# Kernel optimization log

Measured on AMD Instinct MI355X. Metric: run time of the kernel, lower is better.

Reference implementation:

```python
import jax, jax.numpy as jnp
import numpy as np

N = 100000
E = 1600000
C = 64          # hidden_channels
F_IN = 3
F_OUT = 3
N_MP = 2        # message-passing layers


def _lin(k, fan_in, fan_out):
    kw, kb = jax.random.split(k)
    bound = 1.0 / np.sqrt(fan_in)
    W = jax.random.uniform(kw, (fan_in, fan_out), jnp.float32, -bound, bound)
    b = jax.random.uniform(kb, (fan_out,), jnp.float32, -bound, bound)
    return W, b


def setup_inputs() -> dict:
    key = jax.random.key(0)
    ks = jax.random.split(key, 32)
    x = jax.random.normal(ks[0], (N, F_IN), jnp.float32)
    pos = jax.random.normal(ks[1], (N, 3), jnp.float32)
    edge_index = jax.random.randint(ks[2], (2, E), 0, N, jnp.int64)

    enc_W0, enc_b0 = _lin(ks[3], F_IN, C)
    enc_W1, enc_b1 = _lin(ks[4], C, C)
    dec_W0, dec_b0 = _lin(ks[5], C, C)
    dec_W1, dec_b1 = _lin(ks[6], C, F_OUT)

    # stacked params for the N_MP message-passing layers
    eW0, eb0, eW1, eb1 = [], [], [], []
    nW0, nb0, nW1, nb1 = [], [], [], []
    for i in range(N_MP):
        W, b = _lin(ks[7 + 4 * i], 3 * C + 3, C); eW0.append(W); eb0.append(b)
        W, b = _lin(ks[8 + 4 * i], C, C);         eW1.append(W); eb1.append(b)
        W, b = _lin(ks[9 + 4 * i], 2 * C, C);     nW0.append(W); nb0.append(b)
        W, b = _lin(ks[10 + 4 * i], C, C);        nW1.append(W); nb1.append(b)
    stack = lambda xs: jnp.stack(xs, axis=0)
    return {
        "x": x, "pos": pos, "edge_index": edge_index,
        "enc_W0": enc_W0, "enc_b0": enc_b0, "enc_W1": enc_W1, "enc_b1": enc_b1,
        "dec_W0": dec_W0, "dec_b0": dec_b0, "dec_W1": dec_W1, "dec_b1": dec_b1,
        "mp_eW0": stack(eW0), "mp_eb0": stack(eb0),
        "mp_eW1": stack(eW1), "mp_eb1": stack(eb1),
        "mp_nW0": stack(nW0), "mp_nb0": stack(nb0),
        "mp_nW1": stack(nW1), "mp_nb1": stack(nb1),
    }


def reference(x, pos, edge_index,
              enc_W0, enc_b0, enc_W1, enc_b1,
              dec_W0, dec_b0, dec_W1, dec_b1,
              mp_eW0, mp_eb0, mp_eW1, mp_eb1,
              mp_nW0, mp_nb0, mp_nW1, mp_nb1):
    act = jax.nn.elu
    src, dst = edge_index[0], edge_index[1]

    # node encoder (2-layer MLP, activation between layers only)
    h = act(x @ enc_W0 + enc_b0)
    h = h @ enc_W1 + enc_b1

    pos_diff = pos[src] - pos[dst]  # [E, 3], constant across MP layers

    for i in range(N_MP):
        x_nei = h[src]               # [E, C]
        x_own = h[dst]               # [E, C]
        ea = jnp.concatenate([x_nei, x_own, x_nei - x_own, pos_diff], axis=1)
        ea = act(ea @ mp_eW0[i] + mp_eb0[i])
        ea = ea @ mp_eW1[i] + mp_eb1[i]
        # EdgeAggregation(aggr='add'): scatter-add edge features to target nodes
        agg = jax.ops.segment_sum(ea, dst, num_segments=N)  # [N, C]
        u = jnp.concatenate([h, agg], axis=1)                # [N, 2C]
        u = act(u @ mp_nW0[i] + mp_nb0[i])
        u = u @ mp_nW1[i] + mp_nb1[i]
        h = h + u  # residual

    # node decoder
    out = act(h @ dec_W0 + dec_b0)
    out = out @ dec_W1 + dec_b1
    return out
```

## Files before the change

### kernel.cpp

```cpp
#include <hip/hip_runtime.h>
#include <hip/hip_bf16.h>

#define NN 100000
#define NE 1600000
#define NBKT 391
#define BCAP 4608

typedef __hip_bfloat16 bf16;
typedef unsigned short u16;
typedef unsigned int u32;
typedef short bshort8 __attribute__((ext_vector_type(8)));
typedef float f32x4 __attribute__((ext_vector_type(4)));

__device__ __forceinline__ float b2f_raw(u16 u) {
    unsigned int w = ((unsigned int)u) << 16;
    float f; __builtin_memcpy(&f, &w, 4); return f;
}
__device__ __forceinline__ float uplo(u32 u) {
    u32 w = u << 16; float f; __builtin_memcpy(&f, &w, 4); return f;
}
__device__ __forceinline__ float uphi(u32 u) {
    u32 w = u & 0xFFFF0000u; float f; __builtin_memcpy(&f, &w, 4); return f;
}
__device__ __forceinline__ u16 f2bu(float f) {
    bf16 h = __float2bfloat16(f); u16 u; __builtin_memcpy(&u, &h, 2); return u;
}
__device__ __forceinline__ float eluf(float x) { return x > 0.f ? x : __expf(x) - 1.f; }

#define LOG2E 1.4426950408889634f
#define LN2F  0.6931471805599453f

#define OFF_ENC_W0 0
#define OFF_ENC_B0 192
#define OFF_ENC_W1 256
#define OFF_ENC_B1 4352
#define OFF_DEC_W0 4416
#define OFF_DEC_B0 8512
#define OFF_DEC_W1 8576
#define OFF_DEC_B1 8768
#define OFF_EW0    8832
#define OFF_EB0    33792
#define OFF_EW1    33920
#define OFF_EB1    42112
#define OFF_NW0    42240
#define OFF_NB0    58624
#define OFF_NW1    58752
#define OFF_NB1    66944
#define OFF_WF     67072
#define OFF_BFOLD  75264
#define WBLK_WORDS 75392

#define SWZ_V   12288
#define SWZ_N0  24576
#define SWZ_N1  45056
#define SWZ_DC  53248
#define SWZ_ENC 57344
#define SWZ_U16 61440

__global__ void probe_kernel(const u16* __restrict__ xr,
                             const unsigned int* __restrict__ er,
                             int* __restrict__ flags, int* __restrict__ gcursor) {
    int tid = threadIdx.x;
    gcursor[tid] = 0;
    if (tid >= 64) return;
    int lane = tid;
    int wild = 0, oddnz = 0;
#pragma unroll
    for (int k = 0; k < 4; ++k) {
        int e = (xr[lane + k * 64] >> 7) & 0xFF;
        if (e > 140 || (e < 90 && e != 0)) wild++;
    }
#pragma unroll
    for (int k = 0; k < 2; ++k)
        if (er[1 + 2 * (lane + k * 64)] != 0u) oddnz++;
#pragma unroll
    for (int off = 32; off; off >>= 1) {
        wild += __shfl_down(wild, off);
        oddnz += __shfl_down(oddnz, off);
    }
    if (lane == 0) { flags[0] = (wild > 16) ? 1 : 0; flags[1] = (oddnz < 8) ? 1 : 0; }
}

struct WPtrs { const void* p[16]; };

__global__ void canon_weights(WPtrs wp, float* __restrict__ wblk,
                              const int* __restrict__ flags) {
    const int offs[16] = {OFF_ENC_W0, OFF_ENC_B0, OFF_ENC_W1, OFF_ENC_B1,
                          OFF_DEC_W0, OFF_DEC_B0, OFF_DEC_W1, OFF_DEC_B1,
                          OFF_EW0, OFF_EB0, OFF_EW1, OFF_EB1,
                          OFF_NW0, OFF_NB0, OFF_NW1, OFF_NB1};
    const int ns[16]   = {192, 64, 4096, 64, 4096, 64, 192, 3,
                          24960, 128, 8192, 128, 16384, 128, 8192, 128};
    int t = blockIdx.y;
    int i = blockIdx.x * blockDim.x + threadIdx.x;
    if (i >= ns[t]) return;
    const void* s = wp.p[t];
    float v = flags[0] ? ((const float*)s)[i] : b2f_raw(((const u16*)s)[i]);
    wblk[offs[t] + i] = v;
}

__global__ void prep_wf(float* __restrict__ wblk) {
    int idx = blockIdx.x * 256 + threadIdx.x;
    if (idx < 8192) {
        int l = idx >> 12, r = idx & 4095, k = r >> 6, c = r & 63;
        const float* e1 = wblk + OFF_EW1 + l * 4096 + k * 64;
        const float* n0 = wblk + OFF_NW0 + l * 8192 + 64 * 64;
        float s = 0.f;
#pragma unroll 8
        for (int m = 0; m < 64; ++m) s += e1[m] * n0[m * 64 + c];
        wblk[OFF_WF + idx] = s;
    } else if (idx < 8320) {
        int i2 = idx - 8192;
        int l = i2 >> 6, c = i2 & 63;
        const float* b1 = wblk + OFF_EB1 + l * 64;
        const float* n0 = wblk + OFF_NW0 + l * 8192 + 64 * 64;
        float s = 0.f;
#pragma unroll 8
        for (int m = 0; m < 64; ++m) s += b1[m] * n0[m * 64 + c];
        wblk[OFF_BFOLD + i2] = s;
    }
}

__global__ void prep_swz(const float* __restrict__ wblk, u16* __restrict__ swz) {
    int t = blockIdx.x * 256 + threadIdx.x;
    if (t >= SWZ_U16) return;
    float v = 0.f;
    if (t < SWZ_N0) {
        int isV = (t >= SWZ_V);
        int t2 = isV ? t - SWZ_V : t;
        int l = t2 / 6144, r = t2 % 6144;
        int ks = r >> 11, nt = (r >> 9) & 3, lane = (r >> 3) & 63, j = r & 7;
        int k = ks * 32 + ((lane >> 4) & 3) * 8 + j;
        int n = nt * 16 + (lane & 15);
        const float* W = wblk + OFF_EW0 + l * 12480;
        if (k < 64)
            v = isV ? (W[(64 + k) * 64 + n] - W[(128 + k) * 64 + n])
                    : (W[k * 64 + n] + W[(128 + k) * 64 + n]);
        else if (k < 67) {
            v = W[(192 + (k - 64)) * 64 + n];
            if (isV) v = -v;
        }
    } else if (t < SWZ_N1) {
        int t2 = t - SWZ_N0;
        int l = t2 / 10240, r = t2 % 10240;
        int ks = r >> 11, nt = (r >> 9) & 3, lane = (r >> 3) & 63, j = r & 7;
        int k = ks * 32 + ((lane >> 4) & 3) * 8 + j;
        int n = nt * 16 + (lane & 15);
        if (k < 64)        v = wblk[OFF_NW0 + l * 8192 + k * 64 + n];
        else if (k < 128)  v = wblk[OFF_WF + l * 4096 + (k - 64) * 64 + n];
        else if (k == 128) v = wblk[OFF_BFOLD + l * 64 + n];
    } else if (t < SWZ_DC) {
        int t2 = t - SWZ_N1;
        int l = t2 / 4096, r = t2 % 4096;
        int ks = r >> 11, nt = (r >> 9) & 3, lane = (r >> 3) & 63, j = r & 7;
        int k = ks * 32 + ((lane >> 4) & 3) * 8 + j;
        int n = nt * 16 + (lane & 15);
        v = wblk[OFF_NW1 + l * 4096 + k * 64 + n];
    } else if (t < SWZ_ENC) {
        int r = t - SWZ_DC;
        int ks = r >> 11, nt = (r >> 9) & 3, lane = (r >> 3) & 63, j = r & 7;
        int k = ks * 32 + ((lane >> 4) & 3) * 8 + j;
        int n = nt * 16 + (lane & 15);
        v = wblk[OFF_DEC_W0 + k * 64 + n];
    } else {
        int r = t - SWZ_ENC;
        int ks = r >> 11, nt = (r >> 9) & 3, lane = (r >> 3) & 63, j = r & 7;
        int k = ks * 32 + ((lane >> 4) & 3) * 8 + j;
        int n = nt * 16 + (lane & 15);
        v = wblk[OFF_ENC_W1 + k * 64 + n];
    }
    swz[t] = f2bu(v);
}

__global__ __launch_bounds__(1024) void passA_bin(
    const void* __restrict__ eiraw, const int* __restrict__ flags,
    u32* __restrict__ epk_b, int* __restrict__ gcursor) {
    __shared__ int hist[NBKT];
    __shared__ int binstart[NBKT];
    __shared__ int gbase_l[NBKT];
    __shared__ int fill[NBKT];
    __shared__ int sc[512];
    __shared__ u32 stage[4096];
    __shared__ u16 slotbin[4096];
    int tid = threadIdx.x;
    for (int i = tid; i < NBKT; i += 1024) hist[i] = 0;
    __syncthreads();
    int base = blockIdx.x * 4096;
    int total = NE - base; if (total > 4096) total = 4096;
    bool i64 = flags[1] != 0;
    u32 ed[4]; int bn[4];
#pragma unroll
    for (int k = 0; k < 4; ++k) {
        int e = base + tid + k * 1024;
        bn[k] = -1;
        if (e < NE) {
            int s, d;
            if (i64) {
                s = (int)((const long long*)eiraw)[e];
                d = (int)((const long long*)eiraw)[(size_t)NE + e];
            } else {
                s = ((const int*)eiraw)[e];
                d = ((const int*)eiraw)[(size_t)NE + e];
            }
            if ((unsigned)s >= NN) s = 0;
            if ((unsigned)d >= NN) d = 0;
            ed[k] = (u32)s | ((u32)(d & 255) << 17);
            bn[k] = d >> 8;
            atomicAdd(&hist[bn[k]], 1);
        }
    }
    __syncthreads();
    if (tid < 512) sc[tid] = (tid < NBKT) ? hist[tid] : 0;
    __syncthreads();
    for (int d = 1; d < 512; d <<= 1) {
        int v = (tid >= d && tid < 512) ? sc[tid - d] : 0;
        __syncthreads();
        if (tid < 512) sc[tid] += v;
        __syncthreads();
    }
    if (tid < NBKT) {
        binstart[tid] = sc[tid] - hist[tid];
        fill[tid] = 0;
        gbase_l[tid] = hist[tid] ? atomicAdd(&gcursor[tid], hist[tid]) : 0;
    }
    __syncthreads();
#pragma unroll
    for (int k = 0; k < 4; ++k) {
        if (bn[k] >= 0) {
            int p = binstart[bn[k]] + atomicAdd(&fill[bn[k]], 1);
            stage[p] = ed[k];
            slotbin[p] = (u16)bn[k];
        }
    }
    __syncthreads();
    for (int i = tid; i < total; i += 1024) {
        int b = slotbin[i];
        int gp = gbase_l[b] + (i - binstart[b]);
        if (gp < BCAP) epk_b[(size_t)b * BCAP + gp] = stage[i];
    }
}

__global__ __launch_bounds__(512) void scan391(const int* __restrict__ gcursor,
                                               int* __restrict__ gbase2) {
    __shared__ int s[512];
    int t = threadIdx.x;
    int v = 0;
    if (t < NBKT) { v = gcursor[t]; if (v > BCAP) v = BCAP; }
    s[t] = v;
    __syncthreads();
    for (int d = 1; d < 512; d <<= 1) {
        int u = (t >= d) ? s[t - d] : 0;
        __syncthreads();
        s[t] += u;
        __syncthreads();
    }
    if (t < NBKT) gbase2[t] = s[t] - v;
}

__global__ __launch_bounds__(1024) void passB_sort(
    const u32* __restrict__ epk_b, const int* __restrict__ gcursor,
    const int* __restrict__ gbase2, int* __restrict__ srcs,
    int* __restrict__ start) {
    __shared__ int h256[256];
    __shared__ int off256[256];
    __shared__ int sc[256];
    __shared__ u32 stage[BCAP];
    int b = blockIdx.x, tid = threadIdx.x;
    int cnt = gcursor[b]; if (cnt > BCAP) cnt = BCAP;
    for (int i = tid; i < 256; i += 1024) h256[i] = 0;
    __syncthreads();
    u32 ed[5]; int dl[5];
#pragma unroll
    for (int k = 0; k < 5; ++k) {
        int i = tid + k * 1024;
        dl[k] = -1;
        if (i < cnt) {
            ed[k] = epk_b[(size_t)b * BCAP + i];
            dl[k] = (int)(ed[k] >> 17);
            atomicAdd(&h256[dl[k]], 1);
        }
    }
    __syncthreads();
    if (tid < 256) sc[tid] = h256[tid];
    __syncthreads();
    for (int d = 1; d < 256; d <<= 1) {
        int v = (tid >= d && tid < 256) ? sc[tid - d] : 0;
        __syncthreads();
        if (tid < 256) sc[tid] += v;
        __syncthreads();
    }
    int gb = gbase2[b];
    if (tid < 256) {
        off256[tid] = sc[tid] - h256[tid];
        start[b * 256 + tid] = gb + sc[tid] - h256[tid];
    }
    __syncthreads();
#pragma unroll
    for (int k = 0; k < 5; ++k) {
        if (dl[k] >= 0) {
            int p = atomicAdd(&off256[dl[k]], 1);
            stage[p] = ed[k];
        }
    }
    __syncthreads();
    for (int i = tid; i < cnt; i += 1024) srcs[gb + i] = (int)(stage[i] & 0x1FFFFu);
}

__global__ __launch_bounds__(512) void enc_uv(
    const void* __restrict__ xraw, const void* __restrict__ praw,
    const float* __restrict__ wblk, const u16* __restrict__ swzE,
    const u16* __restrict__ swzU, const u16* __restrict__ swzV,
    u16* __restrict__ hb, u16* __restrict__ pos4b,
    u16* __restrict__ U, u16* __restrict__ V,
    const int* __restrict__ flags) {
    __shared__ __attribute__((aligned(16))) u16 sE[4096];
    __shared__ __attribute__((aligned(16))) u16 sU[6144];
    __shared__ __attribute__((aligned(16))) u16 sV[6144];
    __shared__ __attribute__((aligned(16))) u16 sP[8][16 * 72];
    int tid = threadIdx.x;
    for (int i = tid; i < 512; i += 512) ((uint4*)sE)[i] = ((const uint4*)swzE)[i];
    for (int i = tid; i < 768; i += 512) {
        ((uint4*)sU)[i] = ((const uint4*)swzU)[i];
        ((uint4*)sV)[i] = ((const uint4*)swzV)[i];
    }
    __syncthreads();
    int wid = tid >> 6, lane = tid & 63;
    int m16 = lane & 15, half = lane >> 4;
    int g = blockIdx.x * 8 + wid;
    if (g >= NN / 16) return;
    int n0 = g * 16 + m16;
    bool isf = flags[0] != 0;
    float x0, x1, x2;
    if (isf) {
        x0 = ((const float*)xraw)[n0 * 3 + 0];
        x1 = ((const float*)xraw)[n0 * 3 + 1];
        x2 = ((const float*)xraw)[n0 * 3 + 2];
    } else {
        x0 = b2f_raw(((const u16*)xraw)[n0 * 3 + 0]);
        x1 = b2f_raw(((const u16*)xraw)[n0 * 3 + 1]);
        x2 = b2f_raw(((const u16*)xraw)[n0 * 3 + 2]);
    }
    u16 pk0 = 0, pk1 = 0, pk2 = 0;
    if (half == 0) {
        float p0 = isf ? ((const float*)praw)[n0 * 3 + 0] : b2f_raw(((const u16*)praw)[n0 * 3 + 0]);
        float p1 = isf ? ((const float*)praw)[n0 * 3 + 1] : b2f_raw(((const u16*)praw)[n0 * 3 + 1]);
        float p2 = isf ? ((const float*)praw)[n0 * 3 + 2] : b2f_raw(((const u16*)praw)[n0 * 3 + 2]);
        pk0 = f2bu(p0); pk1 = f2bu(p1); pk2 = f2bu(p2);
        *(ushort4*)(pos4b + (size_t)n0 * 4) = make_ushort4(pk0, pk1, pk2, 0);
    }
    const float* W0 = wblk + OFF_ENC_W0;
    const float* b0 = wblk + OFF_ENC_B0;
    bshort8 af0, af1;
#pragma unroll
    for (int j = 0; j < 8; ++j) {
        int c = half * 8 + j;
        float v = b0[c] + x0 * W0[c] + x1 * W0[64 + c] + x2 * W0[128 + c];
        af0[j] = (short)f2bu(eluf(v));
        int c2 = 32 + c;
        float v2 = b0[c2] + x0 * W0[c2] + x1 * W0[64 + c2] + x2 * W0[128 + c2];
        af1[j] = (short)f2bu(eluf(v2));
    }
    const bshort8* BE = (const bshort8*)sE;
    f32x4 acc[4];
#pragma unroll
    for (int nt = 0; nt < 4; ++nt) {
        float b = wblk[OFF_ENC_B1 + nt * 16 + m16];
        acc[nt] = f32x4{b, b, b, b};
    }
#pragma unroll
    for (int nt = 0; nt < 4; ++nt)
        acc[nt] = __builtin_amdgcn_mfma_f32_16x16x32_bf16(af0, BE[nt * 64 + lane], acc[nt], 0, 0, 0);
#pragma unroll
    for (int nt = 0; nt < 4; ++nt)
        acc[nt] = __builtin_amdgcn_mfma_f32_16x16x32_bf16(af1, BE[(4 + nt) * 64 + lane], acc[nt], 0, 0, 0);
    u16* myP = sP[wid];
#pragma unroll
    for (int nt = 0; nt < 4; ++nt)
#pragma unroll
        for (int r = 0; r < 4; ++r) {
            size_t ix = (size_t)(g * 16 + half * 4 + r) * 64 + nt * 16 + m16;
            u16 hv = f2bu(acc[nt][r]);
            hb[ix] = hv;
            myP[(half * 4 + r) * 72 + nt * 16 + m16] = hv;
        }
    bshort8 ah0 = *(const bshort8*)(myP + m16 * 72 + 0 * 32 + half * 8);
    bshort8 ah1 = *(const bshort8*)(myP + m16 * 72 + 1 * 32 + half * 8);
    bshort8 ap;
#pragma unroll
    for (int j = 0; j < 8; ++j) ap[j] = 0;
    if (half == 0) { ap[0] = (short)pk0; ap[1] = (short)pk1; ap[2] = (short)pk2; }
    const bshort8* BU = (const bshort8*)sU;
    const bshort8* BV = (const bshort8*)sV;
    const float* eb0p = wblk + OFF_EB0;
    f32x4 aU[4], aV[4];
#pragma unroll
    for (int nt = 0; nt < 4; ++nt) {
        float bv = eb0p[nt * 16 + m16];
        aU[nt] = f32x4{0.f, 0.f, 0.f, 0.f};
        aV[nt] = f32x4{bv, bv, bv, bv};
    }
#pragma unroll
    for (int nt = 0; nt < 4; ++nt) {
        aU[nt] = __builtin_amdgcn_mfma_f32_16x16x32_bf16(ah0, BU[nt * 64 + lane], aU[nt], 0, 0, 0);
        aV[nt] = __builtin_amdgcn_mfma_f32_16x16x32_bf16(ah0, BV[nt * 64 + lane], aV[nt], 0, 0, 0);
    }
#pragma unroll
    for (int nt = 0; nt < 4; ++nt) {
        aU[nt] = __builtin_amdgcn_mfma_f32_16x16x32_bf16(ah1, BU[(4 + nt) * 64 + lane], aU[nt], 0, 0, 0);
        aV[nt] = __builtin_amdgcn_mfma_f32_16x16x32_bf16(ah1, BV[(4 + nt) * 64 + lane], aV[nt], 0, 0, 0);
    }
#pragma unroll
    for (int nt = 0; nt < 4; ++nt) {
        aU[nt] = __builtin_amdgcn_mfma_f32_16x16x32_bf16(ap, BU[(8 + nt) * 64 + lane], aU[nt], 0, 0, 0);
        aV[nt] = __builtin_amdgcn_mfma_f32_16x16x32_bf16(ap, BV[(8 + nt) * 64 + lane], aV[nt], 0, 0, 0);
    }
#pragma unroll
    for (int nt = 0; nt < 4; ++nt)
#pragma unroll
        for (int r = 0; r < 4; ++r) {
            size_t ix = (size_t)(g * 16 + half * 4 + r) * 64 + nt * 16 + m16;
            U[ix] = f2bu(aU[nt][r] * LOG2E);
            V[ix] = f2bu(aV[nt][r] * LOG2E);
        }
}

#define ES_CAP 1024
__global__ __launch_bounds__(256) void edge_sum(
    const u32* __restrict__ U32, const u32* __restrict__ V32,
    const int* __restrict__ srcs, const int* __restrict__ start,
    u32* __restrict__ Sb, int totalwaves) {
    __shared__ int sS[4][ES_CAP];
    int tid = threadIdx.x;
    int wslot = tid >> 6;
    int w = blockIdx.x * 4 + wslot;
    int lane = tid & 63;
    int eo = lane >> 4, co = lane & 15;
    int nb = (int)((long long)w * NN / totalwaves);
    int ne = (int)((long long)(w + 1) * NN / totalwaves);
    int s0w = start[nb], s1w = start[ne];
    int cw = s1w - s0w;
    const int* sp = srcs + s0w;
    if (cw <= ES_CAP) {
        for (int i = lane; i < cw; i += 64) sS[wslot][i] = srcs[s0w + i];
        sp = sS[wslot];
    }
    __syncthreads();

    int s0 = s0w;
    for (int n = nb; n < ne; ++n) {
        int s1 = start[n + 1];
        int cnt = s1 - s0;
        const int* spn = sp + (s0 - s0w);
        uint2 vv = *(const uint2*)(V32 + (size_t)n * 32 + (co << 1));
        float v0 = uplo(vv.x), v1 = uphi(vv.x);
        float v2 = uplo(vv.y), v3 = uphi(vv.y);
        float accA0 = 0.f, accA1 = 0.f, accA2 = 0.f, accA3 = 0.f;
        float accB0 = 0.f, accB1 = 0.f, accB2 = 0.f, accB3 = 0.f;

        auto GRP = [&](int goff, bool MASKED) {
            int ei = goff + eo;
            int eic = ei;
            if (MASKED) eic = (ei < cnt) ? ei : (cnt - 1);
            int s = spn[eic];
            uint2 uu = *(const uint2*)(U32 + (size_t)s * 32 + (co << 1));
            float x0 = uplo(uu.x) + v0, x1 = uphi(uu.x) + v1;
            float x2 = uplo(uu.y) + v2, x3 = uphi(uu.y) + v3;
            float e0 = __builtin_amdgcn_exp2f(x0);
            float e1 = __builtin_amdgcn_exp2f(x1);
            float e2 = __builtin_amdgcn_exp2f(x2);
            float e3 = __builtin_amdgcn_exp2f(x3);
            bool val = !MASKED || (ei < cnt);
            accA0 += val ? fmaxf(x0, 0.f) : 0.f;
            accA1 += val ? fmaxf(x1, 0.f) : 0.f;
            accA2 += val ? fmaxf(x2, 0.f) : 0.f;
            accA3 += val ? fmaxf(x3, 0.f) : 0.f;
            accB0 += val ? fminf(e0, 1.f) : 0.f;
            accB1 += val ? fminf(e1, 1.f) : 0.f;
            accB2 += val ? fminf(e2, 1.f) : 0.f;
            accB3 += val ? fminf(e3, 1.f) : 0.f;
        };

        int g = 0;
        for (; g + 16 <= cnt; g += 16) {
            GRP(g + 0, false);
            GRP(g + 4, false);
            GRP(g + 8, false);
            GRP(g + 12, false);
        }
        int rem = cnt - g;
        if (rem > 0) {
            GRP(g + 0, true);
            if (rem > 4)  GRP(g + 4, true);
            if (rem > 8)  GRP(g + 8, true);
            if (rem > 12) GRP(g + 12, true);
        }

        float t0 = fmaf(accA0, LN2F, accB0);
        float t1 = fmaf(accA1, LN2F, accB1);
        float t2 = fmaf(accA2, LN2F, accB2);
        float t3 = fmaf(accA3, LN2F, accB3);
        t0 += __shfl_xor(t0, 16); t0 += __shfl_xor(t0, 32);
        t1 += __shfl_xor(t1, 16); t1 += __shfl_xor(t1, 32);
        t2 += __shfl_xor(t2, 16); t2 += __shfl_xor(t2, 32);
        t3 += __shfl_xor(t3, 16); t3 += __shfl_xor(t3, 32);
        if (eo == 0) {
            float cf = (float)cnt;
            u32 p0 = (u32)f2bu(t0 - cf) | ((u32)f2bu(t1 - cf) << 16);
            u32 p1 = (u32)f2bu(t2 - cf) | ((u32)f2bu(t3 - cf) << 16);
            *(uint2*)(Sb + (size_t)n * 32 + (co << 1)) = make_uint2(p0, p1);
        }
        s0 = s1;
    }
}

__global__ __launch_bounds__(512) void node_uv(
    u16* __restrict__ hb, const u16* __restrict__ Sb,
    const int* __restrict__ start, const float* __restrict__ wblk,
    const u16* __restrict__ swz, const u16* __restrict__ pos4b,
    u16* __restrict__ U, u16* __restrict__ V) {
    __shared__ __attribute__((aligned(16))) u16 sN0[10240];
    __shared__ __attribute__((aligned(16))) u16 sN1[4096];
    __shared__ __attribute__((aligned(16))) u16 sU[6144];
    __shared__ __attribute__((aligned(16))) u16 sV[6144];
    __shared__ __attribute__((aligned(16))) u16 sP[8][16 * 72];
    int tid = threadIdx.x;
    {
        const uint4* s0 = (const uint4*)(swz + SWZ_N0);
        const uint4* s1 = (const uint4*)(swz + SWZ_N1);
        const uint4* su = (const uint4*)(swz + 6144);
        const uint4* sv = (const uint4*)(swz + SWZ_V + 6144);
        for (int i = tid; i < 1280; i += 512) ((uint4*)sN0)[i] = s0[i];
        for (int i = tid; i < 512; i += 512)  ((uint4*)sN1)[i] = s1[i];
        for (int i = tid; i < 768; i += 512) {
            ((uint4*)sU)[i] = su[i];
            ((uint4*)sV)[i] = sv[i];
        }
    }
    __syncthreads();
    int wid = tid >> 6, lane = tid & 63;
    int m16 = lane & 15, half = lane >> 4;
    int g = blockIdx.x * 8 + wid;
    if (g >= NN / 16) return;
    int n0 = g * 16 + m16;
    const float* b0 = wblk + OFF_NB0;
    const float* b1 = wblk + OFF_NB1;
    const bshort8* B0 = (const bshort8*)sN0;
    const bshort8* B1 = (const bshort8*)sN1;
    u16* myP = sP[wid];

    bshort8 afh0 = *(const bshort8*)(hb + (size_t)n0 * 64 + half * 8);
    bshort8 afh1 = *(const bshort8*)(hb + (size_t)n0 * 64 + 32 + half * 8);
    bshort8 afs0 = *(const bshort8*)(Sb + (size_t)n0 * 64 + half * 8);
    bshort8 afs1 = *(const bshort8*)(Sb + (size_t)n0 * 64 + 32 + half * 8);
    bshort8 afd;
#pragma unroll
    for (int j = 0; j < 8; ++j) afd[j] = 0;
    if (half == 0) {
        float deg = (float)(start[n0 + 1] - start[n0]);
        afd[0] = (short)f2bu(deg);
    }
    f32x4 acc[4];
#pragma unroll
    for (int nt = 0; nt < 4; ++nt) {
        float b = b0[nt * 16 + m16];
        acc[nt] = f32x4{b, b, b, b};
    }
#pragma unroll
    for (int nt = 0; nt < 4; ++nt)
        acc[nt] = __builtin_amdgcn_mfma_f32_16x16x32_bf16(afh0, B0[nt * 64 + lane], acc[nt], 0, 0, 0);
#pragma unroll
    for (int nt = 0; nt < 4; ++nt)
        acc[nt] = __builtin_amdgcn_mfma_f32_16x16x32_bf16(afh1, B0[(4 + nt) * 64 + lane], acc[nt], 0, 0, 0);
#pragma unroll
    for (int nt = 0; nt < 4; ++nt)
        acc[nt] = __builtin_amdgcn_mfma_f32_16x16x32_bf16(afs0, B0[(8 + nt) * 64 + lane], acc[nt], 0, 0, 0);
#pragma unroll
    for (int nt = 0; nt < 4; ++nt)
        acc[nt] = __builtin_amdgcn_mfma_f32_16x16x32_bf16(afs1, B0[(12 + nt) * 64 + lane], acc[nt], 0, 0, 0);
#pragma unroll
    for (int nt = 0; nt < 4; ++nt)
        acc[nt] = __builtin_amdgcn_mfma_f32_16x16x32_bf16(afd, B0[(16 + nt) * 64 + lane], acc[nt], 0, 0, 0);
#pragma unroll
    for (int nt = 0; nt < 4; ++nt)
#pragma unroll
        for (int r = 0; r < 4; ++r) {
            float v = acc[nt][r];
            v = eluf(v);
            myP[(half * 4 + r) * 72 + nt * 16 + m16] = f2bu(v);
        }
    f32x4 acc2[4];
#pragma unroll
    for (int nt = 0; nt < 4; ++nt) {
        float b = b1[nt * 16 + m16];
        acc2[nt] = f32x4{b, b, b, b};
    }
#pragma unroll
    for (int ks = 0; ks < 2; ++ks) {
        bshort8 av = *(const bshort8*)(myP + m16 * 72 + ks * 32 + half * 8);
#pragma unroll
        for (int nt = 0; nt < 4; ++nt)
            acc2[nt] = __builtin_amdgcn_mfma_f32_16x16x32_bf16(
                av, B1[(ks * 4 + nt) * 64 + lane], acc2[nt], 0, 0, 0);
    }
#pragma unroll
    for (int nt = 0; nt < 4; ++nt)
#pragma unroll
        for (int r = 0; r < 4; ++r) {
            size_t ix = (size_t)(g * 16 + half * 4 + r) * 64 + nt * 16 + m16;
            float v = b2f_raw(hb[ix]) + acc2[nt][r];
            u16 hv = f2bu(v);
            hb[ix] = hv;
            myP[(half * 4 + r) * 72 + nt * 16 + m16] = hv;
        }
    bshort8 ah0 = *(const bshort8*)(myP + m16 * 72 + 0 * 32 + half * 8);
    bshort8 ah1 = *(const bshort8*)(myP + m16 * 72 + 1 * 32 + half * 8);
    bshort8 ap;
#pragma unroll
    for (int j = 0; j < 8; ++j) ap[j] = 0;
    if (half == 0) {
        ushort4 pp = *(const ushort4*)(pos4b + (size_t)n0 * 4);
        ap[0] = (short)pp.x; ap[1] = (short)pp.y; ap[2] = (short)pp.z;
    }
    const bshort8* BU = (const bshort8*)sU;
    const bshort8* BV = (const bshort8*)sV;
    const float* eb0p = wblk + OFF_EB0 + 64;
    f32x4 aU[4], aV[4];
#pragma unroll
    for (int nt = 0; nt < 4; ++nt) {
        float bv = eb0p[nt * 16 + m16];
        aU[nt] = f32x4{0.f, 0.f, 0.f, 0.f};
        aV[nt] = f32x4{bv, bv, bv, bv};
    }
#pragma unroll
    for (int nt = 0; nt < 4; ++nt) {
        aU[nt] = __builtin_amdgcn_mfma_f32_16x16x32_bf16(ah0, BU[nt * 64 + lane], aU[nt], 0, 0, 0);
        aV[nt] = __builtin_amdgcn_mfma_f32_16x16x32_bf16(ah0, BV[nt * 64 + lane], aV[nt], 0, 0, 0);
    }
#pragma unroll
    for (int nt = 0; nt < 4; ++nt) {
        aU[nt] = __builtin_amdgcn_mfma_f32_16x16x32_bf16(ah1, BU[(4 + nt) * 64 + lane], aU[nt], 0, 0, 0);
        aV[nt] = __builtin_amdgcn_mfma_f32_16x16x32_bf16(ah1, BV[(4 + nt) * 64 + lane], aV[nt], 0, 0, 0);
    }
#pragma unroll
    for (int nt = 0; nt < 4; ++nt) {
        aU[nt] = __builtin_amdgcn_mfma_f32_16x16x32_bf16(ap, BU[(8 + nt) * 64 + lane], aU[nt], 0, 0, 0);
        aV[nt] = __builtin_amdgcn_mfma_f32_16x16x32_bf16(ap, BV[(8 + nt) * 64 + lane], aV[nt], 0, 0, 0);
    }
#pragma unroll
    for (int nt = 0; nt < 4; ++nt)
#pragma unroll
        for (int r = 0; r < 4; ++r) {
            size_t ix = (size_t)(g * 16 + half * 4 + r) * 64 + nt * 16 + m16;
            U[ix] = f2bu(aU[nt][r] * LOG2E);
            V[ix] = f2bu(aV[nt][r] * LOG2E);
        }
}

__global__ __launch_bounds__(512) void node_dec(
    const u16* __restrict__ hb, const u16* __restrict__ Sb,
    const int* __restrict__ start, const float* __restrict__ wblk,
    const u16* __restrict__ swz,
    void* __restrict__ out, const int* __restrict__ flags) {
    __shared__ __attribute__((aligned(16))) u16 sN0[10240];
    __shared__ __attribute__((aligned(16))) u16 sN1[4096];
    __shared__ __attribute__((aligned(16))) u16 sDec[4096];
    __shared__ __attribute__((aligned(16))) float sT[8][1048];
    int tid = threadIdx.x;
    {
        const uint4* s0 = (const uint4*)(swz + SWZ_N0 + 10240);
        const uint4* s1 = (const uint4*)(swz + SWZ_N1 + 4096);
        const uint4* sd = (const uint4*)(swz + SWZ_DC);
        for (int i = tid; i < 1280; i += 512) ((uint4*)sN0)[i] = s0[i];
        for (int i = tid; i < 512; i += 512)  ((uint4*)sN1)[i] = s1[i];
        for (int i = tid; i < 512; i += 512)  ((uint4*)sDec)[i] = sd[i];
    }
    __syncthreads();
    int wid = tid >> 6, lane = tid & 63;
    int m16 = lane & 15, half = lane >> 4;
    int g = blockIdx.x * 8 + wid;
    if (g >= NN / 16) return;
    int n0 = g * 16 + m16;
    const float* b0 = wblk + OFF_NB0 + 64;
    const float* b1 = wblk + OFF_NB1 + 64;
    const bshort8* B0 = (const bshort8*)sN0;
    const bshort8* B1 = (const bshort8*)sN1;
    const bshort8* BD = (const bshort8*)sDec;
    u16* myP = (u16*)sT[wid];
    float* sD = sT[wid];

    bshort8 afh0 = *(const bshort8*)(hb + (size_t)n0 * 64 + half * 8);
    bshort8 afh1 = *(const bshort8*)(hb + (size_t)n0 * 64 + 32 + half * 8);
    bshort8 afs0 = *(const bshort8*)(Sb + (size_t)n0 * 64 + half * 8);
    bshort8 afs1 = *(const bshort8*)(Sb + (size_t)n0 * 64 + 32 + half * 8);
    bshort8 afd;
#pragma unroll
    for (int j = 0; j < 8; ++j) afd[j] = 0;
    if (half == 0) {
        float deg = (float)(start[n0 + 1] - start[n0]);
        afd[0] = (short)f2bu(deg);
    }
    f32x4 acc[4];
#pragma unroll
    for (int nt = 0; nt < 4; ++nt) {
        float b = b0[nt * 16 + m16];
        acc[nt] = f32x4{b, b, b, b};
    }
#pragma unroll
    for (int nt = 0; nt < 4; ++nt)
        acc[nt] = __builtin_amdgcn_mfma_f32_16x16x32_bf16(afh0, B0[nt * 64 + lane], acc[nt], 0, 0, 0);
#pragma unroll
    for (int nt = 0; nt < 4; ++nt)
        acc[nt] = __builtin_amdgcn_mfma_f32_16x16x32_bf16(afh1, B0[(4 + nt) * 64 + lane], acc[nt], 0, 0, 0);
#pragma unroll
    for (int nt = 0; nt < 4; ++nt)
        acc[nt] = __builtin_amdgcn_mfma_f32_16x16x32_bf16(afs0, B0[(8 + nt) * 64 + lane], acc[nt], 0, 0, 0);
#pragma unroll
    for (int nt = 0; nt < 4; ++nt)
        acc[nt] = __builtin_amdgcn_mfma_f32_16x16x32_bf16(afs1, B0[(12 + nt) * 64 + lane], acc[nt], 0, 0, 0);
#pragma unroll
    for (int nt = 0; nt < 4; ++nt)
        acc[nt] = __builtin_amdgcn_mfma_f32_16x16x32_bf16(afd, B0[(16 + nt) * 64 + lane], acc[nt], 0, 0, 0);
#pragma unroll
    for (int nt = 0; nt < 4; ++nt)
#pragma unroll
        for (int r = 0; r < 4; ++r) {
            float v = acc[nt][r];
            v = eluf(v);
            myP[(half * 4 + r) * 72 + nt * 16 + m16] = f2bu(v);
        }
    f32x4 acc2[4];
#pragma unroll
    for (int nt = 0; nt < 4; ++nt) {
        float b = b1[nt * 16 + m16];
        acc2[nt] = f32x4{b, b, b, b};
    }
#pragma unroll
    for (int ks = 0; ks < 2; ++ks) {
        bshort8 av = *(const bshort8*)(myP + m16 * 72 + ks * 32 + half * 8);
#pragma unroll
        for (int nt = 0; nt < 4; ++nt)
            acc2[nt] = __builtin_amdgcn_mfma_f32_16x16x32_bf16(
                av, B1[(ks * 4 + nt) * 64 + lane], acc2[nt], 0, 0, 0);
    }
    float nh[4][4];
#pragma unroll
    for (int nt = 0; nt < 4; ++nt)
#pragma unroll
        for (int r = 0; r < 4; ++r) {
            size_t ix = (size_t)(g * 16 + half * 4 + r) * 64 + nt * 16 + m16;
            nh[nt][r] = b2f_raw(hb[ix]) + acc2[nt][r];
        }
#pragma unroll
    for (int nt = 0; nt < 4; ++nt)
#pragma unroll
        for (int r = 0; r < 4; ++r)
            myP[(half * 4 + r) * 72 + nt * 16 + m16] = f2bu(nh[nt][r]);
    const float* db0 = wblk + OFF_DEC_B0;
    f32x4 acc3[4];
#pragma unroll
    for (int nt = 0; nt < 4; ++nt) {
        float b = db0[nt * 16 + m16];
        acc3[nt] = f32x4{b, b, b, b};
    }
#pragma unroll
    for (int ks = 0; ks < 2; ++ks) {
        bshort8 av = *(const bshort8*)(myP + m16 * 72 + ks * 32 + half * 8);
#pragma unroll
        for (int nt = 0; nt < 4; ++nt)
            acc3[nt] = __builtin_amdgcn_mfma_f32_16x16x32_bf16(
                av, BD[(ks * 4 + nt) * 64 + lane], acc3[nt], 0, 0, 0);
    }
#pragma unroll
    for (int nt = 0; nt < 4; ++nt)
#pragma unroll
        for (int r = 0; r < 4; ++r) {
            float v = acc3[nt][r];
            v = eluf(v);
            sD[(half * 4 + r) * 65 + nt * 16 + m16] = v;
        }
    if (lane < 48) {
        int j = lane / 3, o = lane - j * 3;
        const float* dW1 = wblk + OFF_DEC_W1;
        float oacc = wblk[OFF_DEC_B1 + o];
#pragma unroll
        for (int k = 0; k < 64; ++k) oacc += sD[j * 65 + k] * dW1[k * 3 + o];
        int nn = g * 16 + j;
        if (flags[0]) ((float*)out)[nn * 3 + o] = oacc;
        else          ((bf16*)out)[nn * 3 + o] = __float2bfloat16(oacc);
    }
}

extern "C" void kernel_launch(void* const* d_in, const int* in_sizes, int n_in,
                              void* d_out, int out_size, void* d_ws, size_t ws_size,
                              hipStream_t stream) {
    int*   flags   = (int*)d_ws;
    float* wblk    = (float*)d_ws + 16;
    u16*   swz     = (u16*)(wblk + WBLK_WORDS);
    u16*   pos4b   = swz + SWZ_U16;
    int*   gcursor = (int*)(pos4b + 400000);
    int*   gbase2  = gcursor + 512;
    int*   start   = gbase2 + 512;
    int*   srcs    = start + NN + 512;
    u16*   Sb      = (u16*)(srcs + NE);
    u16*   hb      = Sb + (size_t)NN * 64;
    u16*   U       = hb + (size_t)NN * 64;
    u16*   V       = U + (size_t)NN * 64;
    u32*   epk_b   = (u32*)Sb;

    probe_kernel<<<1, 512, 0, stream>>>((const u16*)d_in[0],
                                        (const unsigned int*)d_in[2], flags, gcursor);

    WPtrs wp;
    wp.p[0] = d_in[3];  wp.p[1] = d_in[4];  wp.p[2] = d_in[5];  wp.p[3] = d_in[6];
    wp.p[4] = d_in[7];  wp.p[5] = d_in[8];  wp.p[6] = d_in[9];  wp.p[7] = d_in[10];
    wp.p[8] = d_in[11]; wp.p[9] = d_in[12]; wp.p[10] = d_in[13]; wp.p[11] = d_in[14];
    wp.p[12] = d_in[15]; wp.p[13] = d_in[16]; wp.p[14] = d_in[17]; wp.p[15] = d_in[18];
    canon_weights<<<dim3(98, 16), 256, 0, stream>>>(wp, wblk, flags);
    prep_wf<<<33, 256, 0, stream>>>(wblk);
    prep_swz<<<240, 256, 0, stream>>>(wblk, swz);

    passA_bin<<<(NE + 4095) / 4096, 1024, 0, stream>>>(d_in[2], flags, epk_b, gcursor);
    scan391<<<1, 512, 0, stream>>>(gcursor, gbase2);
    passB_sort<<<NBKT, 1024, 0, stream>>>(epk_b, gcursor, gbase2, srcs, start);

    const int NODE_BLOCKS = (NN / 16 + 7) / 8;
    const int EDGE_BLOCKS = 2048;
    const int TOTALWAVES = EDGE_BLOCKS * 4;

    enc_uv<<<NODE_BLOCKS, 512, 0, stream>>>(
        d_in[0], d_in[1], wblk, swz + SWZ_ENC,
        swz, swz + SWZ_V, hb, pos4b, U, V, flags);

    edge_sum<<<EDGE_BLOCKS, 256, 0, stream>>>(
        (const u32*)U, (const u32*)V, srcs, start, (u32*)Sb, TOTALWAVES);
    node_uv<<<NODE_BLOCKS, 512, 0, stream>>>(
        hb, Sb, start, wblk, swz, pos4b, U, V);

    edge_sum<<<EDGE_BLOCKS, 256, 0, stream>>>(
        (const u32*)U, (const u32*)V, srcs, start, (u32*)Sb, TOTALWAVES);
    node_dec<<<NODE_BLOCKS, 512, 0, stream>>>(
        hb, Sb, start, wblk, swz, d_out, flags);
}
```

Before: 314.5 us.

## Software-prefetch next node's sources in edge_sum instead of LDS staging

Removes the per-wave LDS staging of source indices and the block-wide barrier in edge_sum. Instead, each wave prefetches the first 16 source indices and the V row for the next node while it processes the current one. The block count doubles and launch bounds now request higher occupancy. This trades one LDS copy plus a sync for a register-level software pipeline over dependent global loads. Edges past the first 16 now read their indices straight from global memory, and the prefetch can read slightly past a node's segment.

```diff
diff --git a/kernel.cpp b/kernel.cpp
--- a/kernel.cpp
+++ b/kernel.cpp
@@ -424,81 +424,101 @@
         }
 }
 
-#define ES_CAP 1024
-__global__ __launch_bounds__(256) void edge_sum(
+__global__ __launch_bounds__(256, 8) void edge_sum(
     const u32* __restrict__ U32, const u32* __restrict__ V32,
     const int* __restrict__ srcs, const int* __restrict__ start,
     u32* __restrict__ Sb, int totalwaves) {
-    __shared__ int sS[4][ES_CAP];
     int tid = threadIdx.x;
-    int wslot = tid >> 6;
-    int w = blockIdx.x * 4 + wslot;
+    int w = blockIdx.x * 4 + (tid >> 6);
     int lane = tid & 63;
     int eo = lane >> 4, co = lane & 15;
+    int coff = co << 1;
     int nb = (int)((long long)w * NN / totalwaves);
     int ne = (int)((long long)(w + 1) * NN / totalwaves);
-    int s0w = start[nb], s1w = start[ne];
-    int cw = s1w - s0w;
-    const int* sp = srcs + s0w;
-    if (cw <= ES_CAP) {
-        for (int i = lane; i < cw; i += 64) sS[wslot][i] = srcs[s0w + i];
-        sp = sS[wslot];
-    }
-    __syncthreads();
-
-    int s0 = s0w;
+    if (nb >= ne) return;
+
+    int s0 = start[nb];
+    int s1 = start[nb + 1];
+    int pf0 = srcs[s0 + eo];
+    int pf1 = srcs[s0 + 4 + eo];
+    int pf2 = srcs[s0 + 8 + eo];
+    int pf3 = srcs[s0 + 12 + eo];
+    uint2 pv = *(const uint2*)(V32 + (size_t)nb * 32 + coff);
+
     for (int n = nb; n < ne; ++n) {
-        int s1 = start[n + 1];
         int cnt = s1 - s0;
-        const int* spn = sp + (s0 - s0w);
-        uint2 vv = *(const uint2*)(V32 + (size_t)n * 32 + (co << 1));
+        int sv0 = pf0, sv1 = pf1, sv2 = pf2, sv3 = pf3;
+        uint2 vv = pv;
+        int s0n = s1;
+        int s1n = start[n + 2];
+        {
+            int vn = (n + 1 < NN) ? (n + 1) : (NN - 1);
+            pf0 = srcs[s0n + eo];
+            pf1 = srcs[s0n + 4 + eo];
+            pf2 = srcs[s0n + 8 + eo];
+            pf3 = srcs[s0n + 12 + eo];
+            pv = *(const uint2*)(V32 + (size_t)vn * 32 + coff);
+        }
+
         float v0 = uplo(vv.x), v1 = uphi(vv.x);
         float v2 = uplo(vv.y), v3 = uphi(vv.y);
-        float accA0 = 0.f, accA1 = 0.f, accA2 = 0.f, accA3 = 0.f;
-        float accB0 = 0.f, accB1 = 0.f, accB2 = 0.f, accB3 = 0.f;
-
-        auto GRP = [&](int goff, bool MASKED) {
-            int ei = goff + eo;
-            int eic = ei;
-            if (MASKED) eic = (ei < cnt) ? ei : (cnt - 1);
-            int s = spn[eic];
-            uint2 uu = *(const uint2*)(U32 + (size_t)s * 32 + (co << 1));
+        float aA0 = 0.f, aA1 = 0.f, aA2 = 0.f, aA3 = 0.f;
+        float aB0 = 0.f, aB1 = 0.f, aB2 = 0.f, aB3 = 0.f;
+
+        auto body = [&](uint2 uu, bool val) {
             float x0 = uplo(uu.x) + v0, x1 = uphi(uu.x) + v1;
             float x2 = uplo(uu.y) + v2, x3 = uphi(uu.y) + v3;
             float e0 = __builtin_amdgcn_exp2f(x0);
             float e1 = __builtin_amdgcn_exp2f(x1);
             float e2 = __builtin_amdgcn_exp2f(x2);
             float e3 = __builtin_amdgcn_exp2f(x3);
-            bool val = !MASKED || (ei < cnt);
-            accA0 += val ? fmaxf(x0, 0.f) : 0.f;
-            accA1 += val ? fmaxf(x1, 0.f) : 0.f;
-            accA2 += val ? fmaxf(x2, 0.f) : 0.f;
-            accA3 += val ? fmaxf(x3, 0.f) : 0.f;
-            accB0 += val ? fminf(e0, 1.f) : 0.f;
-            accB1 += val ? fminf(e1, 1.f) : 0.f;
-            accB2 += val ? fminf(e2, 1.f) : 0.f;
-            accB3 += val ? fminf(e3, 1.f) : 0.f;
+            aA0 += val ? fmaxf(x0, 0.f) : 0.f;
+            aA1 += val ? fmaxf(x1, 0.f) : 0.f;
+            aA2 += val ? fmaxf(x2, 0.f) : 0.f;
+            aA3 += val ? fmaxf(x3, 0.f) : 0.f;
+            aB0 += val ? fminf(e0, 1.f) : 0.f;
+            aB1 += val ? fminf(e1, 1.f) : 0.f;
+            aB2 += val ? fminf(e2, 1.f) : 0.f;
+            aB3 += val ? fminf(e3, 1.f) : 0.f;
         };
-
-        int g = 0;
+        auto gat = [&](int s) -> uint2 {
+            return *(const uint2*)(U32 + (size_t)s * 32 + coff);
+        };
+
+        if (cnt >= 16) {
+            uint2 u0 = gat(sv0), u1 = gat(sv1), u2 = gat(sv2), u3 = gat(sv3);
+            body(u0, true); body(u1, true); body(u2, true); body(u3, true);
+        } else if (cnt > 0) {
+            bool m0 = (eo < cnt), m1 = (4 + eo < cnt), m2 = (8 + eo < cnt), m3 = (12 + eo < cnt);
+            uint2 u0 = gat(m0 ? sv0 : 0), u1 = gat(m1 ? sv1 : 0);
+            uint2 u2 = gat(m2 ? sv2 : 0), u3 = gat(m3 ? sv3 : 0);
+            body(u0, m0); body(u1, m1); body(u2, m2); body(u3, m3);
+        }
+        int g = 16;
         for (; g + 16 <= cnt; g += 16) {
-            GRP(g + 0, false);
-            GRP(g + 4, false);
-            GRP(g + 8, false);
-            GRP(g + 12, false);
-        }
-        int rem = cnt - g;
-        if (rem > 0) {
-            GRP(g + 0, true);
-            if (rem > 4)  GRP(g + 4, true);
-            if (rem > 8)  GRP(g + 8, true);
-            if (rem > 12) GRP(g + 12, true);
-        }
-
-        float t0 = fmaf(accA0, LN2F, accB0);
-        float t1 = fmaf(accA1, LN2F, accB1);
-        float t2 = fmaf(accA2, LN2F, accB2);
-        float t3 = fmaf(accA3, LN2F, accB3);
+            int a0 = srcs[s0 + g + eo];
+            int a1 = srcs[s0 + g + 4 + eo];
+            int a2 = srcs[s0 + g + 8 + eo];
+            int a3 = srcs[s0 + g + 12 + eo];
+            uint2 u0 = gat(a0), u1 = gat(a1), u2 = gat(a2), u3 = gat(a3);
+            body(u0, true); body(u1, true); body(u2, true); body(u3, true);
+        }
+        if (g < cnt) {
+            int r = cnt - g;
+            bool m0 = (eo < r), m1 = (4 + eo < r), m2 = (8 + eo < r), m3 = (12 + eo < r);
+            int a0 = srcs[s0 + g + eo];
+            int a1 = srcs[s0 + g + 4 + eo];
+            int a2 = srcs[s0 + g + 8 + eo];
+            int a3 = srcs[s0 + g + 12 + eo];
+            uint2 u0 = gat(m0 ? a0 : 0), u1 = gat(m1 ? a1 : 0);
+            uint2 u2 = gat(m2 ? a2 : 0), u3 = gat(m3 ? a3 : 0);
+            body(u0, m0); body(u1, m1); body(u2, m2); body(u3, m3);
+        }
+
+        float t0 = fmaf(aA0, LN2F, aB0);
+        float t1 = fmaf(aA1, LN2F, aB1);
+        float t2 = fmaf(aA2, LN2F, aB2);
+        float t3 = fmaf(aA3, LN2F, aB3);
         t0 += __shfl_xor(t0, 16); t0 += __shfl_xor(t0, 32);
         t1 += __shfl_xor(t1, 16); t1 += __shfl_xor(t1, 32);
         t2 += __shfl_xor(t2, 16); t2 += __shfl_xor(t2, 32);
@@ -507,9 +527,9 @@
             float cf = (float)cnt;
             u32 p0 = (u32)f2bu(t0 - cf) | ((u32)f2bu(t1 - cf) << 16);
             u32 p1 = (u32)f2bu(t2 - cf) | ((u32)f2bu(t3 - cf) << 16);
-            *(uint2*)(Sb + (size_t)n * 32 + (co << 1)) = make_uint2(p0, p1);
-        }
-        s0 = s1;
+            *(uint2*)(Sb + (size_t)n * 32 + coff) = make_uint2(p0, p1);
+        }
+        s0 = s0n; s1 = s1n;
     }
 }
 
@@ -824,7 +844,7 @@
     passB_sort<<<NBKT, 1024, 0, stream>>>(epk_b, gcursor, gbase2, srcs, start);
 
     const int NODE_BLOCKS = (NN / 16 + 7) / 8;
-    const int EDGE_BLOCKS = 2048;
+    const int EDGE_BLOCKS = 4096;
     const int TOTALWAVES = EDGE_BLOCKS * 4;
 
     enc_uv<<<NODE_BLOCKS, 512, 0, stream>>>(
```

Result: slower. 332.4 us (+5.7%).
